# Performance work log

Hardware: AMD Instinct MI355X
Metric: run time of the kernel (lower is better)

The kernel has to match this reference:

```python
import jax, jax.numpy as jnp
import numpy as np

ALPHA = 0.95
BETA = 0.9

def setup_inputs() -> dict:
    key = jax.random.key(0)
    k1, k2 = jax.random.split(key)
    B, T, I, O = 64, 1000, 512, 256
    inputs = jax.random.normal(k1, (B, T, I), dtype=jnp.float32)
    W = jax.random.normal(k2, (O, I), dtype=jnp.float32) * (1.0 / np.sqrt(I))
    return {"inputs": inputs, "W": W, "nb_steps": T}

def reference(inputs, W, nb_steps):
    B = inputs.shape[0]
    O = W.shape[0]
    # linear projection: h[b,t,o]
    h = jnp.einsum('bti,oi->bto', inputs, W)
    h_t = jnp.swapaxes(h, 0, 1)  # (T, B, O) for scan over time

    def step(carry, ht):
        flt, out = carry
        new_flt = ALPHA * flt + ht
        new_out = BETA * out + flt  # uses OLD flt, matching the torch loop
        return (new_flt, new_out), new_out

    init = (jnp.zeros((B, O), jnp.float32), jnp.zeros((B, O), jnp.float32))
    _, out_rec = jax.lax.scan(step, init, h_t)
    return jnp.swapaxes(out_rec, 0, 1)  # (B, T, O)
```

## Files before the change

### kernel.cpp

```cpp
#include <hip/hip_runtime.h>
#include <stdint.h>


#define ALPHA 0.95f
#define BETA  0.9f

constexpr int Bdim = 64, T = 1000, Idim = 512, Odim = 256;
constexpr int M = Bdim * T;
constexpr int BM = 128, BN = 128, BK = 32;
constexpr int C = 8, L = 125;
constexpr int BO = Bdim * Odim;

typedef short bf16x8 __attribute__((ext_vector_type(8)));
typedef float f32x4  __attribute__((ext_vector_type(4)));

__device__ inline uint32_t pk_bf16(float a, float b) {
  union { float f; uint32_t u; } x, y; x.f = a; y.f = b;
  uint32_t lo = (x.u + 0x7FFFu + ((x.u >> 16) & 1u)) >> 16;
  uint32_t hi = (y.u + 0x7FFFu + ((y.u >> 16) & 1u)) & 0xFFFF0000u;
  return lo | hi;
}
__device__ inline uint16_t f2bf(float a) {
  union { float f; uint32_t u; } x; x.f = a;
  return (uint16_t)((x.u + 0x7FFFu + ((x.u >> 16) & 1u)) >> 16);
}
__device__ inline float bf2f(uint16_t h) {
  union { uint32_t u; float f; } x; x.u = ((uint32_t)h) << 16;
  return x.f;
}

__global__ __launch_bounds__(256) void gemm_h(const float* __restrict__ A,
                                              const float* __restrict__ W,
                                              uint16_t* __restrict__ H) {
  __shared__ uint16_t As[128][40];
  __shared__ uint16_t Bs[128][40];

  const int tid  = threadIdx.x;
  const int lane = tid & 63;
  const int wave = tid >> 6;
  const int wm   = (wave >> 1) * 64;
  const int wn   = (wave & 1) * 64;
  const int l15  = lane & 15;
  const int quad = lane >> 4;
  const int rm   = blockIdx.x * BM;
  const int cn   = blockIdx.y * BN;

  const int sr = tid >> 3;
  const int sc = (tid & 7) * 4;

  f32x4 acc[4][4] = {};

  for (int k0 = 0; k0 < Idim; k0 += BK) {
    __syncthreads();
#pragma unroll
    for (int p = 0; p < 4; ++p) {
      int r = p * 32 + sr;
      const float4 av = *(const float4*)&A[(size_t)(rm + r) * Idim + k0 + sc];
      const float4 bv = *(const float4*)&W[(size_t)(cn + r) * Idim + k0 + sc];
      uint2 ap = make_uint2(pk_bf16(av.x, av.y), pk_bf16(av.z, av.w));
      uint2 bp = make_uint2(pk_bf16(bv.x, bv.y), pk_bf16(bv.z, bv.w));
      *(uint2*)&As[r][sc] = ap;
      *(uint2*)&Bs[r][sc] = bp;
    }
    __syncthreads();

    bf16x8 af[4], bfq[4];
#pragma unroll
    for (int mt = 0; mt < 4; ++mt)
      af[mt] = *(const bf16x8*)&As[wm + mt * 16 + l15][quad * 8];
#pragma unroll
    for (int nt = 0; nt < 4; ++nt)
      bfq[nt] = *(const bf16x8*)&Bs[wn + nt * 16 + l15][quad * 8];
#pragma unroll
    for (int mt = 0; mt < 4; ++mt)
#pragma unroll
      for (int nt = 0; nt < 4; ++nt)
        acc[mt][nt] = __builtin_amdgcn_mfma_f32_16x16x32_bf16(af[mt], bfq[nt], acc[mt][nt], 0, 0, 0);
  }

#pragma unroll
  for (int mt = 0; mt < 4; ++mt) {
#pragma unroll
    for (int nt = 0; nt < 4; ++nt) {
#pragma unroll
      for (int r = 0; r < 4; ++r) {
        int gm = rm + wm + mt * 16 + quad * 4 + r;
        int gn = cn + wn + nt * 16 + l15;
        H[(size_t)gm * Odim + gn] = f2bf(acc[mt][nt][r]);
      }
    }
  }
}

__global__ __launch_bounds__(256) void scan_local(const uint16_t* __restrict__ H,
                                                  float2* __restrict__ St) {
  const int b = blockIdx.x >> 3;
  const int c = blockIdx.x & 7;
  const int o = threadIdx.x;
  const uint16_t* hp = H + ((size_t)(b * T + c * L)) * Odim + o;
  float f = 0.f, u = 0.f;
#pragma unroll 5
  for (int j = 0; j < L; ++j) {
    float hv = bf2f(hp[(size_t)j * Odim]);
    float nu = BETA * u + f;
    f = ALPHA * f + hv;
    u = nu;
  }
  St[c * BO + b * Odim + o] = make_float2(f, u);
}

constexpr double dpow(double x, int n) { double r = 1.0; for (int i = 0; i < n; ++i) r *= x; return r; }

__global__ __launch_bounds__(256) void scan_combine(const float2* __restrict__ St,
                                                    float2* __restrict__ Init) {
  constexpr float AL = (float)dpow(0.95, L);
  constexpr float BL = (float)dpow(0.90, L);
  constexpr float WL = (float)((dpow(0.95, L) - dpow(0.90, L)) / (0.95 - 0.90));
  const int i = blockIdx.x * 256 + threadIdx.x;
  float f = 0.f, u = 0.f;
#pragma unroll
  for (int c = 0; c < C; ++c) {
    Init[c * BO + i] = make_float2(f, u);
    float2 s = St[c * BO + i];
    float nf = AL * f + s.x;
    float nu = BL * u + WL * f + s.y;
    f = nf; u = nu;
  }
}

__global__ __launch_bounds__(256) void scan_final(const uint16_t* __restrict__ H,
                                                  const float2* __restrict__ Init,
                                                  float* __restrict__ Out) {
  const int b = blockIdx.x >> 3;
  const int c = blockIdx.x & 7;
  const int o = threadIdx.x;
  const size_t base = ((size_t)(b * T + c * L)) * Odim + o;
  const uint16_t* hp = H + base;
  float* op = Out + base;
  float2 s = Init[c * BO + b * Odim + o];
  float f = s.x, u = s.y;
#pragma unroll 5
  for (int j = 0; j < L; ++j) {
    float hv = bf2f(hp[(size_t)j * Odim]);
    float nu = BETA * u + f;
    op[(size_t)j * Odim] = nu;
    f = ALPHA * f + hv;
    u = nu;
  }
}

extern "C" void kernel_launch(void* const* d_in, const int* in_sizes, int n_in,
                              void* d_out, int out_size, void* d_ws, size_t ws_size,
                              hipStream_t stream) {
  const float* A = (const float*)d_in[0];
  const float* W = (const float*)d_in[1];
  float* Out = (float*)d_out;

  uint16_t* H = (uint16_t*)d_ws;
  const size_t hbytes = (size_t)M * Odim * sizeof(uint16_t);
  float2* St   = (float2*)((char*)d_ws + hbytes);
  float2* Init = St + (size_t)C * BO;

  dim3 g1(M / BM, Odim / BN);
  gemm_h<<<g1, 256, 0, stream>>>(A, W, H);
  scan_local<<<Bdim * C, 256, 0, stream>>>(H, St);
  scan_combine<<<BO / 256, 256, 0, stream>>>(St, Init);
  scan_final<<<Bdim * C, 256, 0, stream>>>(H, Init, Out);
}
```

Measured before the change: 256.7 us.

## Prefetch GEMM tiles into registers, swizzle LDS, and vectorize chunked scan

The GEMM now loads the next K-tile of A and W into registers while the current tile is being converted and stored. It also packs shared memory as an unpadded XOR-swizzled 128x32 layout with 16-byte stores. The scan kernels cut the time axis into 40 chunks of 25 steps instead of 8 of 125, and each thread handles four output channels with ushort4 loads and float4 stores. Both changes aim to hide global-load latency in the GEMM and to expose more parallelism and wider memory transactions in the scan. The cost is higher register pressure and a longer serial combine over 40 chunks.

```diff
diff --git a/kernel.cpp b/kernel.cpp
--- a/kernel.cpp
+++ b/kernel.cpp
@@ -7,8 +7,7 @@
 
 constexpr int Bdim = 64, T = 1000, Idim = 512, Odim = 256;
 constexpr int M = Bdim * T;
-constexpr int BM = 128, BN = 128, BK = 32;
-constexpr int C = 8, L = 125;
+constexpr int C = 40, L = 25;
 constexpr int BO = Bdim * Odim;
 
 typedef short bf16x8 __attribute__((ext_vector_type(8)));
@@ -32,8 +31,8 @@
 __global__ __launch_bounds__(256) void gemm_h(const float* __restrict__ A,
                                               const float* __restrict__ W,
                                               uint16_t* __restrict__ H) {
-  __shared__ uint16_t As[128][40];
-  __shared__ uint16_t Bs[128][40];
+  __shared__ uint16_t As[128 * 32];
+  __shared__ uint16_t Bs[128 * 32];
 
   const int tid  = threadIdx.x;
   const int lane = tid & 63;
@@ -42,35 +41,61 @@
   const int wn   = (wave & 1) * 64;
   const int l15  = lane & 15;
   const int quad = lane >> 4;
-  const int rm   = blockIdx.x * BM;
-  const int cn   = blockIdx.y * BN;
-
-  const int sr = tid >> 3;
-  const int sc = (tid & 7) * 4;
+  const int rm   = blockIdx.x * 128;
+  const int cn   = blockIdx.y * 128;
+
+  const int srow = tid >> 2;
+  const int sc   = tid & 3;
+  int soff[2];
+#pragma unroll
+  for (int p = 0; p < 2; ++p) {
+    int row = p * 64 + srow;
+    soff[p] = row * 32 + ((sc ^ (row & 3)) * 8);
+  }
+  const float* aB0 = A + (size_t)(rm + srow) * Idim + sc * 8;
+  const float* aB1 = A + (size_t)(rm + 64 + srow) * Idim + sc * 8;
+  const float* bB0 = W + (size_t)(cn + srow) * Idim + sc * 8;
+  const float* bB1 = W + (size_t)(cn + 64 + srow) * Idim + sc * 8;
+
+  const int swz = (quad ^ (l15 & 3)) * 8;
+  int aoff[4], boff[4];
+#pragma unroll
+  for (int t = 0; t < 4; ++t) {
+    aoff[t] = (wm + t * 16 + l15) * 32 + swz;
+    boff[t] = (wn + t * 16 + l15) * 32 + swz;
+  }
 
   f32x4 acc[4][4] = {};
 
-  for (int k0 = 0; k0 < Idim; k0 += BK) {
+  float4 ra0 = *(const float4*)(aB0),     ra1 = *(const float4*)(aB0 + 4);
+  float4 ra2 = *(const float4*)(aB1),     ra3 = *(const float4*)(aB1 + 4);
+  float4 rb0 = *(const float4*)(bB0),     rb1 = *(const float4*)(bB0 + 4);
+  float4 rb2 = *(const float4*)(bB1),     rb3 = *(const float4*)(bB1 + 4);
+
+  for (int k0 = 0; k0 < Idim; k0 += 32) {
     __syncthreads();
-#pragma unroll
-    for (int p = 0; p < 4; ++p) {
-      int r = p * 32 + sr;
-      const float4 av = *(const float4*)&A[(size_t)(rm + r) * Idim + k0 + sc];
-      const float4 bv = *(const float4*)&W[(size_t)(cn + r) * Idim + k0 + sc];
-      uint2 ap = make_uint2(pk_bf16(av.x, av.y), pk_bf16(av.z, av.w));
-      uint2 bp = make_uint2(pk_bf16(bv.x, bv.y), pk_bf16(bv.z, bv.w));
-      *(uint2*)&As[r][sc] = ap;
-      *(uint2*)&Bs[r][sc] = bp;
+    *(uint4*)&As[soff[0]] = make_uint4(pk_bf16(ra0.x, ra0.y), pk_bf16(ra0.z, ra0.w),
+                                       pk_bf16(ra1.x, ra1.y), pk_bf16(ra1.z, ra1.w));
+    *(uint4*)&As[soff[1]] = make_uint4(pk_bf16(ra2.x, ra2.y), pk_bf16(ra2.z, ra2.w),
+                                       pk_bf16(ra3.x, ra3.y), pk_bf16(ra3.z, ra3.w));
+    *(uint4*)&Bs[soff[0]] = make_uint4(pk_bf16(rb0.x, rb0.y), pk_bf16(rb0.z, rb0.w),
+                                       pk_bf16(rb1.x, rb1.y), pk_bf16(rb1.z, rb1.w));
+    *(uint4*)&Bs[soff[1]] = make_uint4(pk_bf16(rb2.x, rb2.y), pk_bf16(rb2.z, rb2.w),
+                                       pk_bf16(rb3.x, rb3.y), pk_bf16(rb3.z, rb3.w));
+    if (k0 + 32 < Idim) {
+      int kn = k0 + 32;
+      ra0 = *(const float4*)(aB0 + kn); ra1 = *(const float4*)(aB0 + kn + 4);
+      ra2 = *(const float4*)(aB1 + kn); ra3 = *(const float4*)(aB1 + kn + 4);
+      rb0 = *(const float4*)(bB0 + kn); rb1 = *(const float4*)(bB0 + kn + 4);
+      rb2 = *(const float4*)(bB1 + kn); rb3 = *(const float4*)(bB1 + kn + 4);
     }
     __syncthreads();
 
     bf16x8 af[4], bfq[4];
 #pragma unroll
-    for (int mt = 0; mt < 4; ++mt)
-      af[mt] = *(const bf16x8*)&As[wm + mt * 16 + l15][quad * 8];
-#pragma unroll
-    for (int nt = 0; nt < 4; ++nt)
-      bfq[nt] = *(const bf16x8*)&Bs[wn + nt * 16 + l15][quad * 8];
+    for (int t = 0; t < 4; ++t) af[t]  = *(const bf16x8*)&As[aoff[t]];
+#pragma unroll
+    for (int t = 0; t < 4; ++t) bfq[t] = *(const bf16x8*)&Bs[boff[t]];
 #pragma unroll
     for (int mt = 0; mt < 4; ++mt)
 #pragma unroll
@@ -79,34 +104,36 @@
   }
 
 #pragma unroll
-  for (int mt = 0; mt < 4; ++mt) {
-#pragma unroll
-    for (int nt = 0; nt < 4; ++nt) {
+  for (int mt = 0; mt < 4; ++mt)
+#pragma unroll
+    for (int nt = 0; nt < 4; ++nt)
 #pragma unroll
       for (int r = 0; r < 4; ++r) {
         int gm = rm + wm + mt * 16 + quad * 4 + r;
         int gn = cn + wn + nt * 16 + l15;
         H[(size_t)gm * Odim + gn] = f2bf(acc[mt][nt][r]);
       }
-    }
-  }
 }
 
 __global__ __launch_bounds__(256) void scan_local(const uint16_t* __restrict__ H,
                                                   float2* __restrict__ St) {
-  const int b = blockIdx.x >> 3;
-  const int c = blockIdx.x & 7;
-  const int o = threadIdx.x;
-  const uint16_t* hp = H + ((size_t)(b * T + c * L)) * Odim + o;
-  float f = 0.f, u = 0.f;
-#pragma unroll 5
+  const int pair = blockIdx.x * 4 + (threadIdx.x >> 6);
+  const int b = pair / C, c = pair % C;
+  const int lane = threadIdx.x & 63;
+  const ushort4* hp = (const ushort4*)(H + (size_t)(b * T + c * L) * Odim) + lane;
+  float f[4] = {}, u[4] = {};
+#pragma unroll
   for (int j = 0; j < L; ++j) {
-    float hv = bf2f(hp[(size_t)j * Odim]);
-    float nu = BETA * u + f;
-    f = ALPHA * f + hv;
-    u = nu;
-  }
-  St[c * BO + b * Odim + o] = make_float2(f, u);
+    ushort4 hv = hp[j * 64];
+    float h0 = bf2f(hv.x), h1 = bf2f(hv.y), h2 = bf2f(hv.z), h3 = bf2f(hv.w);
+    float n0 = BETA * u[0] + f[0]; f[0] = ALPHA * f[0] + h0; u[0] = n0;
+    float n1 = BETA * u[1] + f[1]; f[1] = ALPHA * f[1] + h1; u[1] = n1;
+    float n2 = BETA * u[2] + f[2]; f[2] = ALPHA * f[2] + h2; u[2] = n2;
+    float n3 = BETA * u[3] + f[3]; f[3] = ALPHA * f[3] + h3; u[3] = n3;
+  }
+  float2* sp = &St[(size_t)c * BO + b * Odim + lane * 4];
+#pragma unroll
+  for (int i = 0; i < 4; ++i) sp[i] = make_float2(f[i], u[i]);
 }
 
 constexpr double dpow(double x, int n) { double r = 1.0; for (int i = 0; i < n; ++i) r *= x; return r; }
@@ -120,8 +147,8 @@
   float f = 0.f, u = 0.f;
 #pragma unroll
   for (int c = 0; c < C; ++c) {
-    Init[c * BO + i] = make_float2(f, u);
-    float2 s = St[c * BO + i];
+    Init[(size_t)c * BO + i] = make_float2(f, u);
+    float2 s = St[(size_t)c * BO + i];
     float nf = AL * f + s.x;
     float nu = BL * u + WL * f + s.y;
     f = nf; u = nu;
@@ -131,21 +158,26 @@
 __global__ __launch_bounds__(256) void scan_final(const uint16_t* __restrict__ H,
                                                   const float2* __restrict__ Init,
                                                   float* __restrict__ Out) {
-  const int b = blockIdx.x >> 3;
-  const int c = blockIdx.x & 7;
-  const int o = threadIdx.x;
-  const size_t base = ((size_t)(b * T + c * L)) * Odim + o;
-  const uint16_t* hp = H + base;
-  float* op = Out + base;
-  float2 s = Init[c * BO + b * Odim + o];
-  float f = s.x, u = s.y;
-#pragma unroll 5
+  const int pair = blockIdx.x * 4 + (threadIdx.x >> 6);
+  const int b = pair / C, c = pair % C;
+  const int lane = threadIdx.x & 63;
+  const size_t base = (size_t)(b * T + c * L) * Odim;
+  const ushort4* hp = (const ushort4*)(H + base) + lane;
+  float4* op = (float4*)(Out + base) + lane;
+  const float2* sp = &Init[(size_t)c * BO + b * Odim + lane * 4];
+  float f[4], u[4];
+#pragma unroll
+  for (int i = 0; i < 4; ++i) { float2 s = sp[i]; f[i] = s.x; u[i] = s.y; }
+#pragma unroll
   for (int j = 0; j < L; ++j) {
-    float hv = bf2f(hp[(size_t)j * Odim]);
-    float nu = BETA * u + f;
-    op[(size_t)j * Odim] = nu;
-    f = ALPHA * f + hv;
-    u = nu;
+    ushort4 hv = hp[j * 64];
+    float h0 = bf2f(hv.x), h1 = bf2f(hv.y), h2 = bf2f(hv.z), h3 = bf2f(hv.w);
+    float4 o4;
+    o4.x = BETA * u[0] + f[0]; f[0] = ALPHA * f[0] + h0; u[0] = o4.x;
+    o4.y = BETA * u[1] + f[1]; f[1] = ALPHA * f[1] + h1; u[1] = o4.y;
+    o4.z = BETA * u[2] + f[2]; f[2] = ALPHA * f[2] + h2; u[2] = o4.z;
+    o4.w = BETA * u[3] + f[3]; f[3] = ALPHA * f[3] + h3; u[3] = o4.w;
+    op[j * 64] = o4;
   }
 }
 
@@ -161,9 +193,9 @@
   float2* St   = (float2*)((char*)d_ws + hbytes);
   float2* Init = St + (size_t)C * BO;
 
-  dim3 g1(M / BM, Odim / BN);
+  dim3 g1(M / 128, Odim / 128);
   gemm_h<<<g1, 256, 0, stream>>>(A, W, H);
-  scan_local<<<Bdim * C, 256, 0, stream>>>(H, St);
+  scan_local<<<Bdim * C / 4, 256, 0, stream>>>(H, St);
   scan_combine<<<BO / 256, 256, 0, stream>>>(St, Init);
-  scan_final<<<Bdim * C, 256, 0, stream>>>(H, Init, Out);
-}
+  scan_final<<<Bdim * C / 4, 256, 0, stream>>>(H, Init, Out);
+}
```

After: 250.1 us. 1.03x faster.
